# Kernel tuning notes

Measured on AMD Instinct MI355X. Metric: run time of the kernel, lower is better.

## Reference

```python
import jax, jax.numpy as jnp
import numpy as np

BATCH, SEQ_LEN, D_MODEL, STATE_DIM = 8, 4096, 512, 64
LN_EPS = 1e-5


def _hippo_log_neg_eigs(state_dim):
    A = np.zeros((state_dim, state_dim))
    for i in range(state_dim):
        for j in range(state_dim):
            if i > j:
                A[i, j] = -((2 * i + 1) ** 0.5) * ((2 * j + 1) ** 0.5)
            elif i == j:
                A[i, j] = -(i + 1)
    ev = np.sort(np.linalg.eigvals(A).real)[:state_dim]
    return np.log(-ev + 1e-06).astype(np.float32)


def setup_inputs() -> dict:
    key = jax.random.key(0)
    ks = jax.random.split(key, 8)
    d, s = D_MODEL, STATE_DIM
    return {
        "x": jax.random.normal(ks[0], (BATCH, SEQ_LEN, d), dtype=jnp.float32),
        "log_A": jnp.asarray(_hippo_log_neg_eigs(s)),
        "B": jax.random.normal(ks[1], (d, s), dtype=jnp.float32) * 0.01,
        "C": jax.random.normal(ks[2], (s, d), dtype=jnp.float32) * 0.01,
        "D": jnp.zeros((d,), dtype=jnp.float32),
        "log_dt": jnp.zeros((), dtype=jnp.float32),
        "gamma": jnp.ones((d,), dtype=jnp.float32),
        "beta": jnp.zeros((d,), dtype=jnp.float32),
        "W1": jax.random.normal(ks[3], (d, 2 * d), dtype=jnp.float32) * (1.0 / np.sqrt(d)),
        "b1": jnp.zeros((2 * d,), dtype=jnp.float32),
        "W2": jax.random.normal(ks[4], (2 * d, d), dtype=jnp.float32) * (1.0 / np.sqrt(2 * d)),
        "b2": jnp.zeros((d,), dtype=jnp.float32),
    }


def _layernorm(x, gamma, beta):
    mu = jnp.mean(x, axis=-1, keepdims=True)
    var = jnp.mean(jnp.square(x - mu), axis=-1, keepdims=True)
    return (x - mu) * jax.lax.rsqrt(var + LN_EPS) * gamma + beta


def reference(x, log_A, B, C, D, log_dt, gamma, beta, W1, b1, W2, b2):
    residual = x
    xn = _layernorm(x, gamma, beta)  # [B, L, D]

    dt = jnp.exp(log_dt)
    A_bar = jnp.exp(-jnp.exp(log_A) * dt)  # [S]

    # Precompute input projections for all timesteps, then scan the diagonal recurrence.
    xB = jnp.einsum("bld,ds->lbs", xn, B)  # [L, B, S]
    h0 = jnp.zeros((xn.shape[0], A_bar.shape[0]), dtype=xn.dtype)

    def step(h, xb_t):
        h = A_bar * h + xb_t
        return h, h

    _, hs = jax.lax.scan(step, h0, xB)  # hs: [L, B, S]

    y = jnp.einsum("lbs,sd->bld", hs, C) + xn * D  # [B, L, D]
    y = y + residual

    yn = _layernorm(y, gamma, beta)
    mlp = jax.nn.gelu(yn @ W1 + b1, approximate=False) @ W2 + b2
    return y + mlp
```

## Files before the change

kernel.cpp:

```cpp
#include <hip/hip_runtime.h>
#include <math.h>

#define BATCH 8
#define SEQL 4096
#define DMODEL 512
#define SDIM 64
#define MROWS (BATCH * SEQL)
#define LN_EPS 1e-5f

typedef __attribute__((ext_vector_type(8))) short bf16x8;
typedef __attribute__((ext_vector_type(4))) float f32x4;

__device__ __forceinline__ float wave_sum(float v) {
#pragma unroll
  for (int off = 32; off > 0; off >>= 1) v += __shfl_xor(v, off, 64);
  return v;
}

__device__ __forceinline__ unsigned short f2bf(float f) {
  unsigned int u = __float_as_uint(f);
  u += 0x7fffu + ((u >> 16) & 1u);
  return (unsigned short)(u >> 16);
}

__device__ __forceinline__ float gelu_fast(float v) {
  float s = v * 0.70710678118654752f;
  float ax = fabsf(s);
  float t = 1.0f / (1.0f + 0.3275911f * ax);
  float p = ((((1.061405429f * t - 1.453152027f) * t + 1.421413741f) * t - 0.284496736f) * t +
             0.254829592f) *
            t;
  float er = 1.0f - p * __expf(-ax * ax);
  er = copysignf(er, s);
  return 0.5f * v * (1.0f + er);
}

__device__ __forceinline__ void gl2lds16(const void* g, void* l) {
  __builtin_amdgcn_global_load_lds((const __attribute__((address_space(1))) void*)g,
                                   (__attribute__((address_space(3))) void*)l, 16, 0, 0);
}

__global__ void ln_stats_kernel(const float* __restrict__ x, float* __restrict__ mu,
                                float* __restrict__ rstd, unsigned short* __restrict__ xbf) {
  int row = blockIdx.x * 4 + (threadIdx.x >> 6);
  int lane = threadIdx.x & 63;
  const float4* xp = (const float4*)(x + (size_t)row * DMODEL);
  float4 a = xp[lane * 2];
  float4 b = xp[lane * 2 + 1];
  float s = a.x + a.y + a.z + a.w + b.x + b.y + b.z + b.w;
  float q = a.x * a.x + a.y * a.y + a.z * a.z + a.w * a.w + b.x * b.x + b.y * b.y +
            b.z * b.z + b.w * b.w;
  s = wave_sum(s);
  q = wave_sum(q);
  uint4 pk;
  pk.x = (unsigned)f2bf(a.x) | ((unsigned)f2bf(a.y) << 16);
  pk.y = (unsigned)f2bf(a.z) | ((unsigned)f2bf(a.w) << 16);
  pk.z = (unsigned)f2bf(b.x) | ((unsigned)f2bf(b.y) << 16);
  pk.w = (unsigned)f2bf(b.z) | ((unsigned)f2bf(b.w) << 16);
  ((uint4*)(xbf + (size_t)row * DMODEL))[lane] = pk;
  if (lane == 0) {
    float m = s * (1.0f / DMODEL);
    float var = q * (1.0f / DMODEL) - m * m;
    mu[row] = m;
    rstd[row] = rsqrtf(var + LN_EPS);
  }
}

__device__ __forceinline__ void transpose_body(const float* __restrict__ W,
                                               unsigned short* __restrict__ Wt, int K, int N,
                                               int bx, int by,
                                               unsigned short (*tile)[65]) {
  int k0 = by * 64, n0 = bx * 64;
  int tx = threadIdx.x & 15, ty = threadIdx.x >> 4;
#pragma unroll
  for (int p = 0; p < 4; ++p) {
    int k = p * 16 + ty;
    float4 v = *(const float4*)&W[(size_t)(k0 + k) * N + n0 + tx * 4];
    tile[tx * 4 + 0][k] = f2bf(v.x);
    tile[tx * 4 + 1][k] = f2bf(v.y);
    tile[tx * 4 + 2][k] = f2bf(v.z);
    tile[tx * 4 + 3][k] = f2bf(v.w);
  }
  __syncthreads();
#pragma unroll
  for (int p = 0; p < 4; ++p) {
    int n = p * 16 + ty;
    ushort4 o;
    o.x = tile[n][tx * 4 + 0];
    o.y = tile[n][tx * 4 + 1];
    o.z = tile[n][tx * 4 + 2];
    o.w = tile[n][tx * 4 + 3];
    *(ushort4*)&Wt[(size_t)(n0 + n) * K + k0 + tx * 4] = o;
  }
}

__global__ __launch_bounds__(256) void prep_all_kernel(
    const float* __restrict__ W1, const float* __restrict__ W2, const float* __restrict__ Cm,
    const float* __restrict__ Bm, const float* __restrict__ gamma,
    const float* __restrict__ beta, unsigned short* __restrict__ w1t,
    unsigned short* __restrict__ w2t, unsigned short* __restrict__ ctb,
    unsigned short* __restrict__ Bgt, float* __restrict__ gB, float* __restrict__ bB) {
  __shared__ unsigned short tile[64][65];
  int b = blockIdx.x;
  if (b < 128) {
    transpose_body(W1, w1t, 512, 1024, b & 15, b >> 4, tile);
  } else if (b < 256) {
    transpose_body(W2, w2t, 1024, 512, (b - 128) & 7, (b - 128) >> 3, tile);
  } else if (b < 264) {
    transpose_body(Cm, ctb, 64, 512, b - 256, 0, tile);
  } else {
    int s = (b - 264) * 4 + (threadIdx.x >> 6);
    int l = threadIdx.x & 63;
    float gs = 0.0f, bs = 0.0f;
    unsigned short tmp[8];
#pragma unroll
    for (int u = 0; u < 8; ++u) {
      int d = l * 8 + u;
      float bv = Bm[(size_t)d * SDIM + s];
      float gv = gamma[d], ev = beta[d];
      gs += gv * bv;
      bs += ev * bv;
      tmp[u] = f2bf(gv * bv);
    }
    *(ushort4*)&Bgt[(size_t)s * DMODEL + l * 8] = make_ushort4(tmp[0], tmp[1], tmp[2], tmp[3]);
    *(ushort4*)&Bgt[(size_t)s * DMODEL + l * 8 + 4] =
        make_ushort4(tmp[4], tmp[5], tmp[6], tmp[7]);
    gs = wave_sum(gs);
    bs = wave_sum(bs);
    if (l == 0) {
      gB[s] = gs;
      bB[s] = bs;
    }
  }
}

__global__ __launch_bounds__(256) void xb_mfma_kernel(
    const unsigned short* __restrict__ xbf, const unsigned short* __restrict__ Bgt,
    const float* __restrict__ mu, const float* __restrict__ rstd, const float* __restrict__ gB,
    const float* __restrict__ bB, float* __restrict__ xB) {
  __shared__ unsigned short As[128 * 32];
  __shared__ unsigned short Bs[64 * 32];
  const int t = threadIdx.x;
  const int wave = t >> 6, lane = t & 63;
  const int m0 = blockIdx.x * 128;
  const int wm = wave * 32;
  const int row = t >> 2, seg = t & 3;
  const int fr = lane & 15, fq = lane >> 4;
  f32x4 acc[2][4] = {};
  for (int k0 = 0; k0 < DMODEL; k0 += 32) {
    __syncthreads();
    gl2lds16(xbf + (size_t)(m0 + row) * DMODEL + k0 + seg * 8, As + (size_t)(wave * 16) * 32);
    gl2lds16(xbf + (size_t)(m0 + 64 + row) * DMODEL + k0 + seg * 8,
             As + (size_t)(64 + wave * 16) * 32);
    gl2lds16(Bgt + (size_t)row * DMODEL + k0 + seg * 8, Bs + (size_t)(wave * 16) * 32);
    __syncthreads();
#pragma unroll
    for (int i = 0; i < 2; ++i) {
      bf16x8 a = *(const bf16x8*)&As[(wm + i * 16 + fr) * 32 + fq * 8];
#pragma unroll
      for (int j = 0; j < 4; ++j) {
        bf16x8 b = *(const bf16x8*)&Bs[(j * 16 + fr) * 32 + fq * 8];
        acc[i][j] = __builtin_amdgcn_mfma_f32_16x16x32_bf16(a, b, acc[i][j], 0, 0, 0);
      }
    }
  }
#pragma unroll
  for (int i = 0; i < 2; ++i)
#pragma unroll
    for (int r = 0; r < 4; ++r) {
      const int m = m0 + wm + i * 16 + fq * 4 + r;
      const float rr = rstd[m], negmurr = -mu[m] * rstd[m];
#pragma unroll
      for (int j = 0; j < 4; ++j) {
        const int s = j * 16 + fr;
        xB[(size_t)m * SDIM + s] = rr * acc[i][j][r] + negmurr * gB[s] + bB[s];
      }
    }
}

__global__ void scan_ends_kernel(const float* __restrict__ xB, const float* __restrict__ logA,
                                 const float* __restrict__ logdt, float* __restrict__ ends) {
  int t = blockIdx.x * 256 + threadIdx.x;
  int s = t & 63;
  int c = (t >> 6) & 63;
  int b = t >> 12;
  float a = expf(-expf(logA[s]) * expf(logdt[0]));
  const float* p = xB + ((size_t)(b * SEQL + c * 64)) * SDIM + s;
  float e = 0.0f;
#pragma unroll
  for (int i = 0; i < 64; ++i) e = a * e + p[(size_t)i * SDIM];
  ends[(b * 64 + c) * 64 + s] = e;
}

__global__ void scan_fix_kernel(const float* __restrict__ logA, const float* __restrict__ logdt,
                                const float* __restrict__ ends, const float* __restrict__ xB,
                                unsigned short* __restrict__ hsb) {
  int t = blockIdx.x * 256 + threadIdx.x;
  int s = t & 63;
  int c = (t >> 6) & 63;
  int b = t >> 12;
  float a = expf(-expf(logA[s]) * expf(logdt[0]));
  float a64 = a;
#pragma unroll
  for (int i = 0; i < 6; ++i) a64 *= a64;
  float h = 0.0f;
  for (int cp = 0; cp < c; ++cp) h = a64 * h + ends[(b * 64 + cp) * 64 + s];
  const float* p = xB + ((size_t)(b * SEQL + c * 64)) * SDIM + s;
  unsigned short* q = hsb + ((size_t)(b * SEQL + c * 64)) * SDIM + s;
#pragma unroll
  for (int i = 0; i < 64; ++i) {
    h = a * h + p[(size_t)i * SDIM];
    q[(size_t)i * SDIM] = f2bf(h);
  }
}

__global__ __launch_bounds__(256) void y_gemm_mfma_kernel(
    const unsigned short* __restrict__ hsb, const unsigned short* __restrict__ ctb,
    const float* __restrict__ x, const float* __restrict__ mu1,
    const float* __restrict__ rstd1, const float* __restrict__ gamma,
    const float* __restrict__ beta, const float* __restrict__ Dv, float* __restrict__ out) {
  __shared__ unsigned short As[2 * 128 * 32];
  __shared__ unsigned short Bs[2 * 128 * 32];
  const int t = threadIdx.x;
  const int w = t >> 6, lane = t & 63;
  const int m0 = blockIdx.y * 128, n0 = blockIdx.x * 128;
  const int wm = (w >> 1) * 64, wn = (w & 1) * 64;
  const int fr = lane & 15, fq = lane >> 4;
  const int srow = t >> 2, sseg = t & 3;
#pragma unroll
  for (int h = 0; h < 2; ++h)
#pragma unroll
    for (int c = 0; c < 2; ++c) {
      gl2lds16(hsb + (size_t)(m0 + c * 64 + srow) * SDIM + h * 32 + sseg * 8,
               As + ((size_t)h * 128 + c * 64 + w * 16) * 32);
      gl2lds16(ctb + (size_t)(n0 + c * 64 + srow) * SDIM + h * 32 + sseg * 8,
               Bs + ((size_t)h * 128 + c * 64 + w * 16) * 32);
    }
  __syncthreads();
  f32x4 acc[4][4] = {};
#pragma unroll
  for (int h = 0; h < 2; ++h) {
    bf16x8 a[4], b[4];
#pragma unroll
    for (int i = 0; i < 4; ++i)
      a[i] = *(const bf16x8*)&As[((size_t)h * 128 + wm + i * 16 + fr) * 32 + fq * 8];
#pragma unroll
    for (int j = 0; j < 4; ++j)
      b[j] = *(const bf16x8*)&Bs[((size_t)h * 128 + wn + j * 16 + fr) * 32 + fq * 8];
#pragma unroll
    for (int i = 0; i < 4; ++i)
#pragma unroll
      for (int j = 0; j < 4; ++j)
        acc[i][j] = __builtin_amdgcn_mfma_f32_16x16x32_bf16(a[i], b[j], acc[i][j], 0, 0, 0);
  }
  float mm[4][4], rr[4][4];
#pragma unroll
  for (int i = 0; i < 4; ++i)
#pragma unroll
    for (int r = 0; r < 4; ++r) {
      int m = m0 + wm + i * 16 + fq * 4 + r;
      mm[i][r] = mu1[m];
      rr[i][r] = rstd1[m];
    }
#pragma unroll
  for (int j = 0; j < 4; ++j) {
    const int n = n0 + wn + j * 16 + fr;
    const float ga = gamma[n], be = beta[n], dd = Dv[n];
#pragma unroll
    for (int i = 0; i < 4; ++i) {
      float xv[4];
#pragma unroll
      for (int r = 0; r < 4; ++r)
        xv[r] = x[(size_t)(m0 + wm + i * 16 + fq * 4 + r) * DMODEL + n];
#pragma unroll
      for (int r = 0; r < 4; ++r) {
        float yv = acc[i][j][r] + ((xv[r] - mm[i][r]) * rr[i][r] * ga + be) * dd + xv[r];
        out[(size_t)(m0 + wm + i * 16 + fq * 4 + r) * DMODEL + n] = yv;
      }
    }
  }
}

__global__ void ln_apply_kernel(const float* __restrict__ y, const float* __restrict__ gamma,
                                const float* __restrict__ beta,
                                unsigned short* __restrict__ yn) {
  int row = blockIdx.x * 4 + (threadIdx.x >> 6);
  int lane = threadIdx.x & 63;
  const float4* yp = (const float4*)(y + (size_t)row * DMODEL);
  float4 a = yp[lane * 2];
  float4 b = yp[lane * 2 + 1];
  float s = a.x + a.y + a.z + a.w + b.x + b.y + b.z + b.w;
  float q = a.x * a.x + a.y * a.y + a.z * a.z + a.w * a.w + b.x * b.x + b.y * b.y +
            b.z * b.z + b.w * b.w;
  s = wave_sum(s);
  q = wave_sum(q);
  float m = s * (1.0f / DMODEL);
  float var = q * (1.0f / DMODEL) - m * m;
  float rs = rsqrtf(var + LN_EPS);
  const float4* gp = (const float4*)gamma;
  const float4* bp = (const float4*)beta;
  float4 g0 = gp[lane * 2], g1 = gp[lane * 2 + 1];
  float4 e0 = bp[lane * 2], e1 = bp[lane * 2 + 1];
  float o0x = (a.x - m) * rs * g0.x + e0.x, o0y = (a.y - m) * rs * g0.y + e0.y;
  float o0z = (a.z - m) * rs * g0.z + e0.z, o0w = (a.w - m) * rs * g0.w + e0.w;
  float o1x = (b.x - m) * rs * g1.x + e1.x, o1y = (b.y - m) * rs * g1.y + e1.y;
  float o1z = (b.z - m) * rs * g1.z + e1.z, o1w = (b.w - m) * rs * g1.w + e1.w;
  uint4 pk;
  pk.x = (unsigned)f2bf(o0x) | ((unsigned)f2bf(o0y) << 16);
  pk.y = (unsigned)f2bf(o0z) | ((unsigned)f2bf(o0w) << 16);
  pk.z = (unsigned)f2bf(o1x) | ((unsigned)f2bf(o1y) << 16);
  pk.w = (unsigned)f2bf(o1z) | ((unsigned)f2bf(o1w) << 16);
  ((uint4*)(yn + (size_t)row * DMODEL))[lane] = pk;
}

__global__ __launch_bounds__(256) void mlp1_mfma_kernel(const unsigned short* __restrict__ yn,
                                                        const unsigned short* __restrict__ w1t,
                                                        const float* __restrict__ b1,
                                                        unsigned short* __restrict__ g) {
  __shared__ unsigned short As[128 * 32];
  __shared__ unsigned short Bs[128 * 32];
  const int t = threadIdx.x;
  const int wave = t >> 6, lane = t & 63;
  const int m0 = blockIdx.y * 128, n0 = blockIdx.x * 128;
  const int wm = (wave >> 1) * 64, wn = (wave & 1) * 64;
  const int row0 = t >> 2, seg0 = t & 3;
  const int row1 = (t + 256) >> 2;
  const unsigned short* gA0 = yn + (size_t)(m0 + row0) * 512 + seg0 * 8;
  const unsigned short* gA1 = yn + (size_t)(m0 + row1) * 512 + seg0 * 8;
  const unsigned short* gB0 = w1t + (size_t)(n0 + row0) * 512 + seg0 * 8;
  const unsigned short* gB1 = w1t + (size_t)(n0 + row1) * 512 + seg0 * 8;
  unsigned short* lA0 = As + (size_t)(wave * 64) * 8;
  unsigned short* lA1 = As + (size_t)(256 + wave * 64) * 8;
  unsigned short* lB0 = Bs + (size_t)(wave * 64) * 8;
  unsigned short* lB1 = Bs + (size_t)(256 + wave * 64) * 8;
  f32x4 acc[4][4] = {};
  const int fr = lane & 15, fq = lane >> 4;
  for (int k0 = 0; k0 < 512; k0 += 32) {
    __syncthreads();
    gl2lds16(gA0 + k0, lA0);
    gl2lds16(gA1 + k0, lA1);
    gl2lds16(gB0 + k0, lB0);
    gl2lds16(gB1 + k0, lB1);
    __syncthreads();
#pragma unroll
    for (int i = 0; i < 4; ++i) {
      bf16x8 a = *(const bf16x8*)&As[(wm + i * 16 + fr) * 32 + fq * 8];
#pragma unroll
      for (int j = 0; j < 4; ++j) {
        bf16x8 b = *(const bf16x8*)&Bs[(wn + j * 16 + fr) * 32 + fq * 8];
        acc[i][j] = __builtin_amdgcn_mfma_f32_16x16x32_bf16(a, b, acc[i][j], 0, 0, 0);
      }
    }
  }
#pragma unroll
  for (int i = 0; i < 4; ++i)
#pragma unroll
    for (int j = 0; j < 4; ++j) {
      const int cg = n0 + wn + j * 16 + fr;
      const float bb = b1[cg];
#pragma unroll
      for (int r = 0; r < 4; ++r) {
        const int rg = m0 + wm + i * 16 + fq * 4 + r;
        g[(size_t)rg * 1024 + cg] = f2bf(gelu_fast(acc[i][j][r] + bb));
      }
    }
}

__global__ __launch_bounds__(256) void mlp2_mfma_kernel(const unsigned short* __restrict__ g,
                                                        const unsigned short* __restrict__ w2t,
                                                        const float* __restrict__ b2,
                                                        float* __restrict__ out) {
  __shared__ unsigned short As[128 * 32];
  __shared__ unsigned short Bs[128 * 32];
  const int t = threadIdx.x;
  const int wave = t >> 6, lane = t & 63;
  const int m0 = blockIdx.y * 128, n0 = blockIdx.x * 128;
  const int wm = (wave >> 1) * 64, wn = (wave & 1) * 64;
  const int row0 = t >> 2, seg0 = t & 3;
  const int row1 = (t + 256) >> 2;
  const unsigned short* gA0 = g + (size_t)(m0 + row0) * 1024 + seg0 * 8;
  const unsigned short* gA1 = g + (size_t)(m0 + row1) * 1024 + seg0 * 8;
  const unsigned short* gB0 = w2t + (size_t)(n0 + row0) * 1024 + seg0 * 8;
  const unsigned short* gB1 = w2t + (size_t)(n0 + row1) * 1024 + seg0 * 8;
  unsigned short* lA0 = As + (size_t)(wave * 64) * 8;
  unsigned short* lA1 = As + (size_t)(256 + wave * 64) * 8;
  unsigned short* lB0 = Bs + (size_t)(wave * 64) * 8;
  unsigned short* lB1 = Bs + (size_t)(256 + wave * 64) * 8;
  f32x4 acc[4][4] = {};
  const int fr = lane & 15, fq = lane >> 4;
  for (int k0 = 0; k0 < 1024; k0 += 32) {
    __syncthreads();
    gl2lds16(gA0 + k0, lA0);
    gl2lds16(gA1 + k0, lA1);
    gl2lds16(gB0 + k0, lB0);
    gl2lds16(gB1 + k0, lB1);
    __syncthreads();
#pragma unroll
    for (int i = 0; i < 4; ++i) {
      bf16x8 a = *(const bf16x8*)&As[(wm + i * 16 + fr) * 32 + fq * 8];
#pragma unroll
      for (int j = 0; j < 4; ++j) {
        bf16x8 b = *(const bf16x8*)&Bs[(wn + j * 16 + fr) * 32 + fq * 8];
        acc[i][j] = __builtin_amdgcn_mfma_f32_16x16x32_bf16(a, b, acc[i][j], 0, 0, 0);
      }
    }
  }
#pragma unroll
  for (int i = 0; i < 4; ++i)
#pragma unroll
    for (int j = 0; j < 4; ++j) {
      const int cg = n0 + wn + j * 16 + fr;
      const float bb = b2[cg];
#pragma unroll
      for (int r = 0; r < 4; ++r) {
        const int rg = m0 + wm + i * 16 + fq * 4 + r;
        const size_t off = (size_t)rg * 512 + cg;
        out[off] = out[off] + acc[i][j][r] + bb;
      }
    }
}

extern "C" void kernel_launch(void* const* d_in, const int* in_sizes, int n_in, void* d_out,
                              int out_size, void* d_ws, size_t ws_size, hipStream_t stream) {
  const float* x = (const float*)d_in[0];
  const float* logA = (const float*)d_in[1];
  const float* Bm = (const float*)d_in[2];
  const float* Cm = (const float*)d_in[3];
  const float* Dv = (const float*)d_in[4];
  const float* logdt = (const float*)d_in[5];
  const float* gamma = (const float*)d_in[6];
  const float* beta = (const float*)d_in[7];
  const float* W1 = (const float*)d_in[8];
  const float* b1 = (const float*)d_in[9];
  const float* W2 = (const float*)d_in[10];
  const float* b2 = (const float*)d_in[11];
  float* out = (float*)d_out;

  char* ws = (char*)d_ws;
  float* mu1 = (float*)(ws + 0);
  float* rstd1 = (float*)(ws + 131072);
  float* ends = (float*)(ws + 262144);
  float* gB = (float*)(ws + 524288);
  float* bB = (float*)(ws + 524800);
  unsigned short* Bgt = (unsigned short*)(ws + 525312);
  unsigned short* ctb = (unsigned short*)(ws + 590848);
  unsigned short* w1t = (unsigned short*)(ws + 656384);
  unsigned short* w2t = (unsigned short*)(ws + 1704960);
  unsigned short* g = (unsigned short*)(ws + 2753536);
  unsigned short* xbf = (unsigned short*)(ws + 2753536);
  float* xB = (float*)(ws + 69862400);
  unsigned short* hsb = (unsigned short*)(ws + 78251008);
  unsigned short* yn = (unsigned short*)(ws + 82445312);

  prep_all_kernel<<<280, 256, 0, stream>>>(W1, W2, Cm, Bm, gamma, beta, w1t, w2t, ctb, Bgt, gB,
                                           bB);
  ln_stats_kernel<<<MROWS / 4, 256, 0, stream>>>(x, mu1, rstd1, xbf);
  xb_mfma_kernel<<<MROWS / 128, 256, 0, stream>>>(xbf, Bgt, mu1, rstd1, gB, bB, xB);
  scan_ends_kernel<<<128, 256, 0, stream>>>(xB, logA, logdt, ends);
  scan_fix_kernel<<<128, 256, 0, stream>>>(logA, logdt, ends, xB, hsb);
  y_gemm_mfma_kernel<<<dim3(DMODEL / 128, MROWS / 128), 256, 0, stream>>>(
      hsb, ctb, x, mu1, rstd1, gamma, beta, Dv, out);
  ln_apply_kernel<<<MROWS / 4, 256, 0, stream>>>(out, gamma, beta, yn);
  mlp1_mfma_kernel<<<dim3(1024 / 128, MROWS / 128), 256, 0, stream>>>(yn, w1t, b1, g);
  mlp2_mfma_kernel<<<dim3(512 / 128, MROWS / 128), 256, 0, stream>>>(g, w2t, b2, out);
}
```

Before: 347.1 us.

## Replace MLP GEMMs with 256x256 double-buffered swizzled pipelined MFMA kernel

Replaces the two 128x128 single-buffered MLP GEMM kernels with one templated 256x256-tile kernel using 8 waves, BK=64, double-buffered LDS with XOR swizzling, and global-to-LDS prefetch interleaved with MFMA phases under explicit waitcnt/barrier control and s_setprio. The aim is to raise data reuse per tile, remove LDS bank conflicts, and hide global load latency behind compute. It uses 128 KB of LDS per block and many accumulator registers, and depends on hand-tuned vmcnt counts being correct.

Result: faster. 322.3 us (-7.1%).

```diff
diff --git a/kernel.cpp b/kernel.cpp
--- a/kernel.cpp
+++ b/kernel.cpp
@@ -313,109 +313,115 @@
   ((uint4*)(yn + (size_t)row * DMODEL))[lane] = pk;
 }
 
-__global__ __launch_bounds__(256) void mlp1_mfma_kernel(const unsigned short* __restrict__ yn,
-                                                        const unsigned short* __restrict__ w1t,
-                                                        const float* __restrict__ b1,
-                                                        unsigned short* __restrict__ g) {
-  __shared__ unsigned short As[128 * 32];
-  __shared__ unsigned short Bs[128 * 32];
+template <int K, int NALL, int EPI>
+__global__ __launch_bounds__(512, 2) void gemm256_kernel(
+    const unsigned short* __restrict__ Am, const unsigned short* __restrict__ Bm,
+    const float* __restrict__ bias, unsigned short* __restrict__ gout,
+    float* __restrict__ out) {
+  __shared__ alignas(16) unsigned short As[2][256 * 64];
+  __shared__ alignas(16) unsigned short Bs[2][256 * 64];
   const int t = threadIdx.x;
-  const int wave = t >> 6, lane = t & 63;
-  const int m0 = blockIdx.y * 128, n0 = blockIdx.x * 128;
-  const int wm = (wave >> 1) * 64, wn = (wave & 1) * 64;
-  const int row0 = t >> 2, seg0 = t & 3;
-  const int row1 = (t + 256) >> 2;
-  const unsigned short* gA0 = yn + (size_t)(m0 + row0) * 512 + seg0 * 8;
-  const unsigned short* gA1 = yn + (size_t)(m0 + row1) * 512 + seg0 * 8;
-  const unsigned short* gB0 = w1t + (size_t)(n0 + row0) * 512 + seg0 * 8;
-  const unsigned short* gB1 = w1t + (size_t)(n0 + row1) * 512 + seg0 * 8;
-  unsigned short* lA0 = As + (size_t)(wave * 64) * 8;
-  unsigned short* lA1 = As + (size_t)(256 + wave * 64) * 8;
-  unsigned short* lB0 = Bs + (size_t)(wave * 64) * 8;
-  unsigned short* lB1 = Bs + (size_t)(256 + wave * 64) * 8;
-  f32x4 acc[4][4] = {};
+  const int wid = t >> 6, lane = t & 63;
+  const int m0 = blockIdx.y * 256, n0 = blockIdx.x * 256;
+  const int wm = (wid >> 2) * 128, wn = (wid & 3) * 64;
   const int fr = lane & 15, fq = lane >> 4;
-  for (int k0 = 0; k0 < 512; k0 += 32) {
-    __syncthreads();
-    gl2lds16(gA0 + k0, lA0);
-    gl2lds16(gA1 + k0, lA1);
-    gl2lds16(gB0 + k0, lB0);
-    gl2lds16(gB1 + k0, lB1);
-    __syncthreads();
-#pragma unroll
-    for (int i = 0; i < 4; ++i) {
-      bf16x8 a = *(const bf16x8*)&As[(wm + i * 16 + fr) * 32 + fq * 8];
-#pragma unroll
-      for (int j = 0; j < 4; ++j) {
-        bf16x8 b = *(const bf16x8*)&Bs[(wn + j * 16 + fr) * 32 + fq * 8];
-        acc[i][j] = __builtin_amdgcn_mfma_f32_16x16x32_bf16(a, b, acc[i][j], 0, 0, 0);
-      }
-    }
-  }
-#pragma unroll
-  for (int i = 0; i < 4; ++i)
+  constexpr int NT = K / 64;
+  const int srow = t >> 3;
+  const int ksw = ((t & 7) ^ ((t >> 3) & 7)) << 3;
+
+  auto stageA = [&](int bb, int h, int kt) {
+    const unsigned short* s0 = Am + (size_t)(m0 + h * 128 + srow) * K + kt * 64 + ksw;
+    gl2lds16(s0, &As[bb][(h * 128 + wid * 8) * 64]);
+    gl2lds16(s0 + (size_t)64 * K, &As[bb][(h * 128 + 64 + wid * 8) * 64]);
+  };
+  auto stageB = [&](int bb, int h, int kt) {
+    const unsigned short* s0 = Bm + (size_t)(n0 + h * 128 + srow) * K + kt * 64 + ksw;
+    gl2lds16(s0, &Bs[bb][(h * 128 + wid * 8) * 64]);
+    gl2lds16(s0 + (size_t)64 * K, &Bs[bb][(h * 128 + 64 + wid * 8) * 64]);
+  };
+  auto LDA = [&](int bb, int i, int s) -> bf16x8 {
+    const int row = wm + i * 16 + fr;
+    const int slot = (s * 4 + fq) ^ (fr & 7);
+    return *(const bf16x8*)&As[bb][row * 64 + slot * 8];
+  };
+  auto LDB = [&](int bb, int j, int s) -> bf16x8 {
+    const int col = wn + j * 16 + fr;
+    const int slot = (s * 4 + fq) ^ (fr & 7);
+    return *(const bf16x8*)&Bs[bb][col * 64 + slot * 8];
+  };
+
+  stageA(0, 0, 0);
+  stageA(0, 1, 0);
+  stageB(0, 0, 0);
+  stageB(0, 1, 0);
+  stageB(1, 0, 1);
+  stageB(1, 1, 1);
+  asm volatile("s_waitcnt vmcnt(4)" ::: "memory");
+  asm volatile("s_barrier" ::: "memory");
+
+  f32x4 acc[8][4] = {};
+  for (int c = 0; c < NT; ++c) {
+    const int b = c & 1;
+    bf16x8 bfr[2][4];
+#pragma unroll
+    for (int q = 0; q < 4; ++q) {
+      bf16x8 a2[2][2];
+#pragma unroll
+      for (int ii = 0; ii < 2; ++ii)
+#pragma unroll
+        for (int s = 0; s < 2; ++s) a2[ii][s] = LDA(b, 2 * q + ii, s);
+      if (q == 0) {
+#pragma unroll
+        for (int s = 0; s < 2; ++s)
+#pragma unroll
+          for (int j = 0; j < 4; ++j) bfr[s][j] = LDB(b, j, s);
+        if (c + 1 < NT) stageA(b ^ 1, 0, c + 1);
+      } else if (q == 1) {
+        if (c + 1 < NT) stageA(b ^ 1, 1, c + 1);
+      } else if (q == 2) {
+        asm volatile("" ::: "memory");
+        if (c + 2 < NT) stageB(b, 0, c + 2);
+      } else {
+        if (c + 2 < NT) stageB(b, 1, c + 2);
+      }
+      asm volatile("s_barrier" ::: "memory");
+      __builtin_amdgcn_s_setprio(1);
+#pragma unroll
+      for (int ii = 0; ii < 2; ++ii)
+#pragma unroll
+        for (int s = 0; s < 2; ++s)
+#pragma unroll
+          for (int j = 0; j < 4; ++j)
+            acc[2 * q + ii][j] = __builtin_amdgcn_mfma_f32_16x16x32_bf16(
+                a2[ii][s], bfr[s][j], acc[2 * q + ii][j], 0, 0, 0);
+      __builtin_amdgcn_s_setprio(0);
+      if (q < 3) {
+        asm volatile("s_barrier" ::: "memory");
+      } else if (c < NT - 1) {
+        if (c < NT - 2)
+          asm volatile("s_waitcnt vmcnt(4)" ::: "memory");
+        else
+          asm volatile("s_waitcnt vmcnt(0)" ::: "memory");
+        asm volatile("s_barrier" ::: "memory");
+      }
+    }
+  }
+
+#pragma unroll
+  for (int i = 0; i < 8; ++i)
 #pragma unroll
     for (int j = 0; j < 4; ++j) {
       const int cg = n0 + wn + j * 16 + fr;
-      const float bb = b1[cg];
+      const float bb = bias[cg];
 #pragma unroll
       for (int r = 0; r < 4; ++r) {
         const int rg = m0 + wm + i * 16 + fq * 4 + r;
-        g[(size_t)rg * 1024 + cg] = f2bf(gelu_fast(acc[i][j][r] + bb));
-      }
-    }
-}
-
-__global__ __launch_bounds__(256) void mlp2_mfma_kernel(const unsigned short* __restrict__ g,
-                                                        const unsigned short* __restrict__ w2t,
-                                                        const float* __restrict__ b2,
-                                                        float* __restrict__ out) {
-  __shared__ unsigned short As[128 * 32];
-  __shared__ unsigned short Bs[128 * 32];
-  const int t = threadIdx.x;
-  const int wave = t >> 6, lane = t & 63;
-  const int m0 = blockIdx.y * 128, n0 = blockIdx.x * 128;
-  const int wm = (wave >> 1) * 64, wn = (wave & 1) * 64;
-  const int row0 = t >> 2, seg0 = t & 3;
-  const int row1 = (t + 256) >> 2;
-  const unsigned short* gA0 = g + (size_t)(m0 + row0) * 1024 + seg0 * 8;
-  const unsigned short* gA1 = g + (size_t)(m0 + row1) * 1024 + seg0 * 8;
-  const unsigned short* gB0 = w2t + (size_t)(n0 + row0) * 1024 + seg0 * 8;
-  const unsigned short* gB1 = w2t + (size_t)(n0 + row1) * 1024 + seg0 * 8;
-  unsigned short* lA0 = As + (size_t)(wave * 64) * 8;
-  unsigned short* lA1 = As + (size_t)(256 + wave * 64) * 8;
-  unsigned short* lB0 = Bs + (size_t)(wave * 64) * 8;
-  unsigned short* lB1 = Bs + (size_t)(256 + wave * 64) * 8;
-  f32x4 acc[4][4] = {};
-  const int fr = lane & 15, fq = lane >> 4;
-  for (int k0 = 0; k0 < 1024; k0 += 32) {
-    __syncthreads();
-    gl2lds16(gA0 + k0, lA0);
-    gl2lds16(gA1 + k0, lA1);
-    gl2lds16(gB0 + k0, lB0);
-    gl2lds16(gB1 + k0, lB1);
-    __syncthreads();
-#pragma unroll
-    for (int i = 0; i < 4; ++i) {
-      bf16x8 a = *(const bf16x8*)&As[(wm + i * 16 + fr) * 32 + fq * 8];
-#pragma unroll
-      for (int j = 0; j < 4; ++j) {
-        bf16x8 b = *(const bf16x8*)&Bs[(wn + j * 16 + fr) * 32 + fq * 8];
-        acc[i][j] = __builtin_amdgcn_mfma_f32_16x16x32_bf16(a, b, acc[i][j], 0, 0, 0);
-      }
-    }
-  }
-#pragma unroll
-  for (int i = 0; i < 4; ++i)
-#pragma unroll
-    for (int j = 0; j < 4; ++j) {
-      const int cg = n0 + wn + j * 16 + fr;
-      const float bb = b2[cg];
-#pragma unroll
-      for (int r = 0; r < 4; ++r) {
-        const int rg = m0 + wm + i * 16 + fq * 4 + r;
-        const size_t off = (size_t)rg * 512 + cg;
-        out[off] = out[off] + acc[i][j][r] + bb;
+        if (EPI == 0) {
+          gout[(size_t)rg * NALL + cg] = f2bf(gelu_fast(acc[i][j][r] + bb));
+        } else {
+          const size_t off = (size_t)rg * NALL + cg;
+          out[off] = out[off] + acc[i][j][r] + bb;
+        }
       }
     }
 }
@@ -461,6 +467,8 @@
   y_gemm_mfma_kernel<<<dim3(DMODEL / 128, MROWS / 128), 256, 0, stream>>>(
       hsb, ctb, x, mu1, rstd1, gamma, beta, Dv, out);
   ln_apply_kernel<<<MROWS / 4, 256, 0, stream>>>(out, gamma, beta, yn);
-  mlp1_mfma_kernel<<<dim3(1024 / 128, MROWS / 128), 256, 0, stream>>>(yn, w1t, b1, g);
-  mlp2_mfma_kernel<<<dim3(512 / 128, MROWS / 128), 256, 0, stream>>>(g, w2t, b2, out);
-}
+  gemm256_kernel<512, 1024, 0><<<dim3(1024 / 256, MROWS / 256), 512, 0, stream>>>(
+      yn, w1t, b1, g, nullptr);
+  gemm256_kernel<1024, 512, 1><<<dim3(512 / 256, MROWS / 256), 512, 0, stream>>>(
+      g, w2t, b2, nullptr, out);
+}
```
